# Performance work log

Measured on AMD Instinct MI355X. Metric: run time of the kernel, lower is better.

The kernel has to match this reference:

```python
import jax, jax.numpy as jnp
import numpy as np

EMB_DIM = 1024
N_HEADS = 16
HEAD_DIM = EMB_DIM // N_HEADS
WINDOW = 128
B, T = 4, 2048


def setup_inputs() -> dict:
    key = jax.random.key(0)
    k1, k2, k3 = jax.random.split(key, 3)
    x = jax.random.normal(k1, (B, T, EMB_DIM), dtype=jnp.float32)
    # nn.Linear weights: stored as [out, in], applied as x @ W^T
    s1 = 1.0 / np.sqrt(EMB_DIM)
    w_qkv = jax.random.uniform(k2, (3 * EMB_DIM, EMB_DIM), jnp.float32, -s1, s1)
    w_out = jax.random.uniform(k3, (EMB_DIM, EMB_DIM), jnp.float32, -s1, s1)
    return {"x": x, "w_qkv": w_qkv, "w_out": w_out}


def reference(x, w_qkv, w_out):
    Bs, Ts, C = x.shape
    scale = HEAD_DIM ** -0.5
    qkv = x @ w_qkv.T                                   # [B,T,3C]
    qkv = qkv.reshape(Bs, Ts, 3, N_HEADS, HEAD_DIM)
    qkv = jnp.transpose(qkv, (2, 0, 3, 1, 4))           # [3,B,H,T,D]
    q, k, v = qkv[0], qkv[1], qkv[2]
    scores = jnp.einsum('bhtd,bhsd->bhts', q, k) * scale  # [B,H,T,T]
    i = jnp.arange(Ts)[:, None]
    j = jnp.arange(Ts)[None, :]
    # causal AND within sliding window: i - WINDOW <= j <= i
    allowed = (j <= i) & (j >= i - WINDOW)               # [T,T] bool
    scores = jnp.where(allowed[None, None], scores, -jnp.inf)
    attn = jax.nn.softmax(scores, axis=-1)
    out = jnp.einsum('bhts,bhsd->bhtd', attn, v)         # [B,H,T,D]
    out = jnp.transpose(out, (0, 2, 1, 3)).reshape(Bs, Ts, C)
    return out @ w_out.T
```

## Files before the change

kernel.cpp:

```cpp
#include <hip/hip_runtime.h>
#include <hip/hip_bf16.h>
#include <stdint.h>

typedef __attribute__((ext_vector_type(8))) short bf16x8;
typedef __attribute__((ext_vector_type(4))) float f32x4;
typedef __attribute__((ext_vector_type(4))) unsigned short u16x4;

#define B_ 4
#define T_ 2048
#define C_ 1024
#define H_ 16
#define D_ 64

__device__ __forceinline__ unsigned short f2bf(float f) {
  union { float f; uint32_t u; } v; v.f = f;
  uint32_t u = v.u;
  uint32_t r = (u + 0x7FFFu + ((u >> 16) & 1u)) >> 16;
  return (unsigned short)r;
}

__global__ void __launch_bounds__(256) cast_all(const float* __restrict__ x,
                                                const float* __restrict__ wqkv,
                                                const float* __restrict__ wout,
                                                unsigned short* __restrict__ xb,
                                                unsigned short* __restrict__ wqkvb,
                                                unsigned short* __restrict__ woutb) {
  int bid = blockIdx.x;
  const float* src; unsigned short* dst; int i;
  if (bid < 8192)       { src = x;    dst = xb;    i = bid * 256 + threadIdx.x; }
  else if (bid < 11264) { src = wqkv; dst = wqkvb; i = (bid - 8192) * 256 + threadIdx.x; }
  else                  { src = wout; dst = woutb; i = (bid - 11264) * 256 + threadIdx.x; }
  float4 f = ((const float4*)src)[i];
  u16x4 o;
  o[0] = f2bf(f.x); o[1] = f2bf(f.y); o[2] = f2bf(f.z); o[3] = f2bf(f.w);
  ((u16x4*)dst)[i] = o;
}

__global__ void __launch_bounds__(256, 2) gemm_qkv(const unsigned short* __restrict__ A,
                                                   const unsigned short* __restrict__ Bm,
                                                   unsigned short* __restrict__ qb,
                                                   unsigned short* __restrict__ kb,
                                                   unsigned short* __restrict__ vb) {
  __shared__ short lds[24576];
  const int tid = threadIdx.x;
  const int bm = blockIdx.y * 256;
  const int bn = blockIdx.x * 128;

  const int wave = tid >> 6;
  const int l = tid & 63;
  const int wm = wave >> 1, wn = wave & 1;
  const int lm = l & 15, lq = l >> 4;
  const int lr = l >> 2;
  const int lc = (l & 3) << 3;

  f32x4 acc[8][4];
#pragma unroll
  for (int i = 0; i < 8; i++)
#pragma unroll
    for (int j = 0; j < 4; j++) acc[i][j] = (f32x4){0.f, 0.f, 0.f, 0.f};

  const unsigned short* gs[6];
  int ldo[6];
#pragma unroll
  for (int i = 0; i < 6; i++) {
    int c = wave * 6 + i;
    if (c < 16) {
      gs[i] = A + (size_t)(bm + 16 * c + lr) * 1024 + lc;
      ldo[i] = c * 512;
    } else {
      gs[i] = Bm + (size_t)(bn + 16 * (c - 16) + lr) * 1024 + lc;
      ldo[i] = 8192 + (c - 16) * 512;
    }
  }

#define STAGE(curb, kk)                                                          \
  do {                                                                           \
    _Pragma("unroll")                                                            \
    for (int i = 0; i < 6; i++) {                                                \
      __builtin_amdgcn_global_load_lds(                                          \
          (__attribute__((address_space(1))) void*)(uintptr_t)(const void*)(gs[i] + (kk)), \
          (__attribute__((address_space(3))) void*)(lds + ldo[i] + (curb) * 12288),        \
          16, 0, 0);                                                             \
    }                                                                            \
  } while (0)

  STAGE(0, 0);
  int cur = 0;
  __syncthreads();

  for (int k0 = 0; k0 < 1024; k0 += 32) {
    if (k0 + 32 < 1024) STAGE(cur ^ 1, k0 + 32);
    const short* As_ = lds + cur * 12288;
    const short* Bs_ = lds + cur * 12288 + 8192;
    bf16x8 Bf[4];
#pragma unroll
    for (int j = 0; j < 4; j++)
      Bf[j] = *(const bf16x8*)&Bs_[(wn * 64 + 16 * j + lm) * 32 + 8 * lq];
#pragma unroll
    for (int h = 0; h < 2; h++) {
      bf16x8 Af[4];
#pragma unroll
      for (int i = 0; i < 4; i++)
        Af[i] = *(const bf16x8*)&As_[(wm * 128 + 64 * h + 16 * i + lm) * 32 + 8 * lq];
#pragma unroll
      for (int i = 0; i < 4; i++)
#pragma unroll
        for (int j = 0; j < 4; j++)
          acc[4 * h + i][j] =
              __builtin_amdgcn_mfma_f32_16x16x32_bf16(Af[i], Bf[j], acc[4 * h + i][j], 0, 0, 0);
    }
    __syncthreads();
    cur ^= 1;
  }
#undef STAGE

  if (bn >= 2048) {
#pragma unroll
    for (int h = 0; h < 2; h++)
#pragma unroll
      for (int i = 0; i < 4; i++)
#pragma unroll
        for (int j = 0; j < 4; j++) {
          int m0 = bm + wm * 128 + 64 * h + 16 * i + 4 * lq;
          int n = (bn - 2048) + wn * 64 + 16 * j + lm;
          int hh = n >> 6, d = n & 63;
          int b = m0 >> 11, t = m0 & 2047;
          u16x4 o;
#pragma unroll
          for (int r = 0; r < 4; r++) o[r] = f2bf(acc[4 * h + i][j][r]);
          *(u16x4*)&vb[(((size_t)(b * 16 + hh)) * 64 + d) * 2048 + t] = o;
        }
  } else {
#pragma unroll
    for (int p = 0; p < 2; ++p) {
      if (p) __syncthreads();
      if (wm == p) {
#pragma unroll
        for (int h = 0; h < 2; h++)
#pragma unroll
          for (int i = 0; i < 4; i++)
#pragma unroll
            for (int j = 0; j < 4; j++)
#pragma unroll
              for (int r = 0; r < 4; r++)
                lds[(64 * h + 16 * i + 4 * lq + r) * 132 + wn * 64 + 16 * j + lm] =
                    (short)f2bf(acc[4 * h + i][j][r]);
      }
      __syncthreads();
#pragma unroll
      for (int k = 0; k < 8; k++) {
        int c = tid + 256 * k;
        int row = c >> 4;
        int col = (c & 15) << 3;
        bf16x8 v = *(const bf16x8*)&lds[row * 132 + col];
        int m = bm + 128 * p + row, n = bn + col;
        int which = n >> 10, rem = n & 1023;
        int hh = rem >> 6, d = rem & 63;
        int b = m >> 11, t = m & 2047;
        unsigned short* dst = (which == 0) ? qb : kb;
        *(bf16x8*)&dst[(((size_t)(b * 16 + hh)) * 2048 + t) * 64 + d] = v;
      }
    }
  }
}

__global__ void __launch_bounds__(256) gemm_out(const unsigned short* __restrict__ A,
                                                const unsigned short* __restrict__ Bm,
                                                float* __restrict__ fo) {
  __shared__ short lds[16384];
  const int tid = threadIdx.x;
  const int bm = blockIdx.y * 128;
  const int bn = blockIdx.x * 128;
  const int wave = tid >> 6;
  const int l = tid & 63;
  const int wm = wave >> 1, wn = wave & 1;
  const int lm = l & 15, lq = l >> 4;
  const int lr = l >> 2;
  const int lc = (l & 3) << 3;

  f32x4 acc[4][4];
#pragma unroll
  for (int i = 0; i < 4; i++)
#pragma unroll
    for (int j = 0; j < 4; j++) acc[i][j] = (f32x4){0.f, 0.f, 0.f, 0.f};

  const unsigned short* gsrc[4];
  int ldoff[4];
#pragma unroll
  for (int i = 0; i < 4; i++) {
    int c = wave * 4 + i;
    if (c < 8) {
      gsrc[i] = A + (size_t)(bm + 16 * c + lr) * 1024 + lc;
      ldoff[i] = (16 * c) * 32;
    } else {
      gsrc[i] = Bm + (size_t)(bn + 16 * (c - 8) + lr) * 1024 + lc;
      ldoff[i] = 8192 + (16 * (c - 8)) * 32;
    }
  }

#define STAGE(curb, kk)                                                          \
  do {                                                                           \
    _Pragma("unroll")                                                            \
    for (int i = 0; i < 4; i++) {                                                \
      __builtin_amdgcn_global_load_lds(                                          \
          (__attribute__((address_space(1))) void*)(uintptr_t)(const void*)(gsrc[i] + (kk)), \
          (__attribute__((address_space(3))) void*)(lds + ldoff[i] + (curb) * 4096),         \
          16, 0, 0);                                                             \
    }                                                                            \
  } while (0)

  STAGE(0, 0);
  int cur = 0;
  __syncthreads();

  for (int k0 = 0; k0 < 1024; k0 += 32) {
    if (k0 + 32 < 1024) STAGE(cur ^ 1, k0 + 32);
    bf16x8 af[4], bfr[4];
#pragma unroll
    for (int i = 0; i < 4; i++)
      af[i] = *(const bf16x8*)&lds[cur * 4096 + (wm * 64 + 16 * i + lm) * 32 + 8 * lq];
#pragma unroll
    for (int j = 0; j < 4; j++)
      bfr[j] = *(const bf16x8*)&lds[8192 + cur * 4096 + (wn * 64 + 16 * j + lm) * 32 + 8 * lq];
#pragma unroll
    for (int i = 0; i < 4; i++)
#pragma unroll
      for (int j = 0; j < 4; j++)
        acc[i][j] = __builtin_amdgcn_mfma_f32_16x16x32_bf16(af[i], bfr[j], acc[i][j], 0, 0, 0);
    __syncthreads();
    cur ^= 1;
  }
#undef STAGE

#pragma unroll
  for (int i = 0; i < 4; i++)
#pragma unroll
    for (int j = 0; j < 4; j++)
#pragma unroll
      for (int r = 0; r < 4; r++) {
        int m = bm + wm * 64 + 16 * i + 4 * lq + r;
        int n = bn + wn * 64 + 16 * j + lm;
        fo[(size_t)m * 1024 + n] = acc[i][j][r];
      }
}

__global__ void __launch_bounds__(256, 4) attn_swa(const unsigned short* __restrict__ Qb,
                                                   const unsigned short* __restrict__ Kb,
                                                   const unsigned short* __restrict__ Vt,
                                                   unsigned short* __restrict__ Ob) {
  __shared__ short P[4][16 * 48];
  const int wv = threadIdx.x >> 6;
  const int l = threadIdx.x & 63;
  const int wid = blockIdx.x * 4 + wv;
  const int bh = wid >> 6;
  const int t0 = (wid & 63) << 5;
  const int lm = l & 15, lq = l >> 4;
  const size_t base = (size_t)bh * (T_ * D_);

  bf16x8 qf[2][2];
#pragma unroll
  for (int qt = 0; qt < 2; qt++) {
    qf[qt][0] = *(const bf16x8*)(Qb + base + (size_t)(t0 + 16 * qt + lm) * 64 + 8 * lq);
    qf[qt][1] = *(const bf16x8*)(Qb + base + (size_t)(t0 + 16 * qt + lm) * 64 + 32 + 8 * lq);
  }

  float mst[2] = {-1e30f, -1e30f}, lst[2] = {0.f, 0.f};
  f32x4 Oa[2][4];
#pragma unroll
  for (int qt = 0; qt < 2; qt++)
#pragma unroll
    for (int jt = 0; jt < 4; jt++) Oa[qt][jt] = (f32x4){0.f, 0.f, 0.f, 0.f};

  const float cs = 0.125f * 1.44269504f;
  int jstart = t0 - 128; if (jstart < 0) jstart = 0;

  for (int j0 = jstart; j0 < t0 + 32; j0 += 32) {
    bf16x8 ka[2][2];
#pragma unroll
    for (int hh = 0; hh < 2; hh++) {
      int kr = j0 + 16 * hh + lm;
      ka[hh][0] = *(const bf16x8*)(Kb + base + (size_t)kr * 64 + 8 * lq);
      ka[hh][1] = *(const bf16x8*)(Kb + base + (size_t)kr * 64 + 32 + 8 * lq);
    }
    bf16x8 vf[4];
#pragma unroll
    for (int jt = 0; jt < 4; jt++)
      vf[jt] = *(const bf16x8*)(Vt + base + (size_t)(16 * jt + lm) * 2048 + j0 + 8 * lq);

#pragma unroll
    for (int qt = 0; qt < 2; qt++) {
      const int t0q = t0 + 16 * qt;
      const int t = t0q + lm;
      f32x4 s0 = (f32x4){0.f, 0.f, 0.f, 0.f}, s1 = (f32x4){0.f, 0.f, 0.f, 0.f};
      s0 = __builtin_amdgcn_mfma_f32_16x16x32_bf16(ka[0][0], qf[qt][0], s0, 0, 0, 0);
      s0 = __builtin_amdgcn_mfma_f32_16x16x32_bf16(ka[0][1], qf[qt][1], s0, 0, 0, 0);
      s1 = __builtin_amdgcn_mfma_f32_16x16x32_bf16(ka[1][0], qf[qt][0], s1, 0, 0, 0);
      s1 = __builtin_amdgcn_mfma_f32_16x16x32_bf16(ka[1][1], qf[qt][1], s1, 0, 0, 0);
      float sv[8];
      float m2 = -1e30f;
#pragma unroll
      for (int hh = 0; hh < 2; hh++)
#pragma unroll
        for (int r = 0; r < 4; r++) {
          int k = j0 + 16 * hh + 4 * lq + r;
          float x = (hh ? s1[r] : s0[r]) * cs;
          bool okm = (k <= t) && (k + 128 >= t);
          sv[hh * 4 + r] = okm ? x : -1e30f;
          m2 = fmaxf(m2, sv[hh * 4 + r]);
        }
      m2 = fmaxf(m2, __shfl_xor(m2, 16));
      m2 = fmaxf(m2, __shfl_xor(m2, 32));
      float mn = fmaxf(mst[qt], m2);
      float a = __builtin_amdgcn_exp2f(mst[qt] - mn);
      float ps = 0.f;
#pragma unroll
      for (int i = 0; i < 8; i++) {
        sv[i] = (sv[i] > -1e29f) ? __builtin_amdgcn_exp2f(sv[i] - mn) : 0.f;
        ps += sv[i];
      }
      ps += __shfl_xor(ps, 16);
      ps += __shfl_xor(ps, 32);
      lst[qt] = lst[qt] * a + ps;
      mst[qt] = mn;
#pragma unroll
      for (int hh = 0; hh < 2; hh++) {
        u16x4 pk;
#pragma unroll
        for (int r = 0; r < 4; r++) pk[r] = f2bf(sv[hh * 4 + r]);
        *(u16x4*)&P[wv][lm * 48 + 16 * hh + 4 * lq] = pk;
      }
      float al[4];
#pragma unroll
      for (int r = 0; r < 4; r++) al[r] = __shfl(a, 4 * lq + r);
#pragma unroll
      for (int jt = 0; jt < 4; jt++)
#pragma unroll
        for (int r = 0; r < 4; r++) Oa[qt][jt][r] *= al[r];
      bf16x8 pa = *(const bf16x8*)&P[wv][lm * 48 + 8 * lq];
#pragma unroll
      for (int jt = 0; jt < 4; jt++)
        Oa[qt][jt] = __builtin_amdgcn_mfma_f32_16x16x32_bf16(pa, vf[jt], Oa[qt][jt], 0, 0, 0);
    }
  }
  const int b = bh >> 4, h = bh & 15;
#pragma unroll
  for (int qt = 0; qt < 2; qt++) {
    float inv = 1.0f / lst[qt];
    float invl[4];
#pragma unroll
    for (int r = 0; r < 4; r++) invl[r] = __shfl(inv, 4 * lq + r);
#pragma unroll
    for (int r = 0; r < 4; r++) {
      int t = t0 + 16 * qt + 4 * lq + r;
#pragma unroll
      for (int jt = 0; jt < 4; jt++) {
        int c = h * 64 + 16 * jt + lm;
        Ob[((size_t)(b * T_ + t)) * 1024 + c] = f2bf(Oa[qt][jt][r] * invl[r]);
      }
    }
  }
}

extern "C" void kernel_launch(void* const* d_in, const int* in_sizes, int n_in,
                              void* d_out, int out_size, void* d_ws, size_t ws_size,
                              hipStream_t stream) {
  const float* x = (const float*)d_in[0];
  const float* w_qkv = (const float*)d_in[1];
  const float* w_out = (const float*)d_in[2];
  float* out = (float*)d_out;

  unsigned short* xb = (unsigned short*)d_ws;
  unsigned short* wqkvb = xb + (size_t)8192 * 1024;
  unsigned short* woutb = wqkvb + (size_t)3072 * 1024;
  unsigned short* qb = woutb + (size_t)1024 * 1024;
  unsigned short* kb = qb + (size_t)64 * 2048 * 64;
  unsigned short* vb = kb + (size_t)64 * 2048 * 64;

  cast_all<<<12288, 256, 0, stream>>>(x, w_qkv, w_out, xb, wqkvb, woutb);

  gemm_qkv<<<dim3(24, 32), 256, 0, stream>>>(xb, wqkvb, qb, kb, vb);

  attn_swa<<<1024, 256, 0, stream>>>(qb, kb, vb, xb);

  gemm_out<<<dim3(8, 64), 256, 0, stream>>>(xb, woutb, out);
}
```

Before: 216.4 us.

## Rewrite QKV GEMM as 8-wave 256x256 tile with 4-stage LDS pipeline

The QKV projection GEMM moves from 256-thread blocks with 256x128 tiles and double buffering to 512-thread blocks with 256x256 tiles. It uses a 4-deep LDS ring buffer whose A and B stages are issued at separate points in the loop, controlled with explicit vmcnt/lgkmcnt waits, raw s_barrier, sched_barrier fences and setprio around the MFMA bursts. The goal is more operand reuse per LDS load and better overlap of global-to-LDS copies with matrix math. In exchange it uses 128KB of LDS per block, which may limit occupancy to one block per CU, and relies on fragile hand-counted wait counts.

```diff
diff --git a/kernel.cpp b/kernel.cpp
--- a/kernel.cpp
+++ b/kernel.cpp
@@ -36,22 +36,20 @@
   ((u16x4*)dst)[i] = o;
 }
 
-__global__ void __launch_bounds__(256, 2) gemm_qkv(const unsigned short* __restrict__ A,
-                                                   const unsigned short* __restrict__ Bm,
-                                                   unsigned short* __restrict__ qb,
-                                                   unsigned short* __restrict__ kb,
-                                                   unsigned short* __restrict__ vb) {
-  __shared__ short lds[24576];
+__global__ void __launch_bounds__(512, 2) gemm_qkv8(const unsigned short* __restrict__ A,
+                                                    const unsigned short* __restrict__ Bm,
+                                                    unsigned short* __restrict__ qb,
+                                                    unsigned short* __restrict__ kb,
+                                                    unsigned short* __restrict__ vb) {
+  __shared__ short lds[65536];
   const int tid = threadIdx.x;
   const int bm = blockIdx.y * 256;
-  const int bn = blockIdx.x * 128;
-
+  const int bn = blockIdx.x * 256;
   const int wave = tid >> 6;
   const int l = tid & 63;
-  const int wm = wave >> 1, wn = wave & 1;
+  const int wr = wave >> 2;
+  const int wc = wave & 3;
   const int lm = l & 15, lq = l >> 4;
-  const int lr = l >> 2;
-  const int lc = (l & 3) << 3;
 
   f32x4 acc[8][4];
 #pragma unroll
@@ -59,109 +57,135 @@
 #pragma unroll
     for (int j = 0; j < 4; j++) acc[i][j] = (f32x4){0.f, 0.f, 0.f, 0.f};
 
-  const unsigned short* gs[6];
-  int ldo[6];
-#pragma unroll
-  for (int i = 0; i < 6; i++) {
-    int c = wave * 6 + i;
-    if (c < 16) {
-      gs[i] = A + (size_t)(bm + 16 * c + lr) * 1024 + lc;
-      ldo[i] = c * 512;
-    } else {
-      gs[i] = Bm + (size_t)(bn + 16 * (c - 16) + lr) * 1024 + lc;
-      ldo[i] = 8192 + (c - 16) * 512;
-    }
-  }
-
-#define STAGE(curb, kk)                                                          \
+  const unsigned short* gA[2];
+  const unsigned short* gB[2];
+  int dA[2], dB[2];
+#pragma unroll
+  for (int i = 0; i < 2; i++) {
+    int c = i * 512 + tid;
+    gA[i] = A + (size_t)(bm + (c >> 2)) * 1024 + (c & 3) * 8;
+    gB[i] = Bm + (size_t)(bn + (c >> 2)) * 1024 + (c & 3) * 8;
+    dA[i] = c * 8;
+    dB[i] = 8192 + c * 8;
+  }
+
+#define STA(t)                                                                   \
   do {                                                                           \
     _Pragma("unroll")                                                            \
-    for (int i = 0; i < 6; i++) {                                                \
+    for (int i = 0; i < 2; i++)                                                  \
       __builtin_amdgcn_global_load_lds(                                          \
-          (__attribute__((address_space(1))) void*)(uintptr_t)(const void*)(gs[i] + (kk)), \
-          (__attribute__((address_space(3))) void*)(lds + ldo[i] + (curb) * 12288),        \
+          (__attribute__((address_space(1))) void*)(uintptr_t)(const void*)(gA[i] + (t) * 32), \
+          (__attribute__((address_space(3))) void*)(lds + ((t) & 3) * 16384 + dA[i]),          \
           16, 0, 0);                                                             \
-    }                                                                            \
   } while (0)
-
-  STAGE(0, 0);
-  int cur = 0;
-  __syncthreads();
-
-  for (int k0 = 0; k0 < 1024; k0 += 32) {
-    if (k0 + 32 < 1024) STAGE(cur ^ 1, k0 + 32);
-    const short* As_ = lds + cur * 12288;
-    const short* Bs_ = lds + cur * 12288 + 8192;
-    bf16x8 Bf[4];
-#pragma unroll
-    for (int j = 0; j < 4; j++)
-      Bf[j] = *(const bf16x8*)&Bs_[(wn * 64 + 16 * j + lm) * 32 + 8 * lq];
-#pragma unroll
-    for (int h = 0; h < 2; h++) {
-      bf16x8 Af[4];
-#pragma unroll
-      for (int i = 0; i < 4; i++)
-        Af[i] = *(const bf16x8*)&As_[(wm * 128 + 64 * h + 16 * i + lm) * 32 + 8 * lq];
-#pragma unroll
-      for (int i = 0; i < 4; i++)
-#pragma unroll
-        for (int j = 0; j < 4; j++)
-          acc[4 * h + i][j] =
-              __builtin_amdgcn_mfma_f32_16x16x32_bf16(Af[i], Bf[j], acc[4 * h + i][j], 0, 0, 0);
-    }
-    __syncthreads();
-    cur ^= 1;
-  }
-#undef STAGE
+#define STB(t)                                                                   \
+  do {                                                                           \
+    _Pragma("unroll")                                                            \
+    for (int i = 0; i < 2; i++)                                                  \
+      __builtin_amdgcn_global_load_lds(                                          \
+          (__attribute__((address_space(1))) void*)(uintptr_t)(const void*)(gB[i] + (t) * 32), \
+          (__attribute__((address_space(3))) void*)(lds + ((t) & 3) * 16384 + dB[i]),          \
+          16, 0, 0);                                                             \
+  } while (0)
+#define FENCE() __builtin_amdgcn_sched_barrier(0)
+
+  STA(0); STB(0); STA(1); STB(1);
+  FENCE();
+
+  for (int t = 0; t < 32; ++t) {
+    const short* Sa = lds + (t & 3) * 16384;
+    const short* Sb = Sa + 8192;
+    if (t + 2 < 32) STA(t + 2);
+    FENCE();
+    if (t <= 29)      asm volatile("s_waitcnt vmcnt(6)" ::: "memory");
+    else if (t == 30) asm volatile("s_waitcnt vmcnt(4)" ::: "memory");
+    else              asm volatile("s_waitcnt vmcnt(0)" ::: "memory");
+    __builtin_amdgcn_s_barrier();
+    FENCE();
+    bf16x8 Af[8], Bf[2];
+#pragma unroll
+    for (int mi = 0; mi < 8; mi++)
+      Af[mi] = *(const bf16x8*)&Sa[(wr * 128 + 16 * mi + lm) * 32 + 8 * lq];
+#pragma unroll
+    for (int nj = 0; nj < 2; nj++)
+      Bf[nj] = *(const bf16x8*)&Sb[(wc * 64 + 16 * nj + lm) * 32 + 8 * lq];
+    asm volatile("s_waitcnt lgkmcnt(0)" ::: "memory");
+    FENCE();
+    __builtin_amdgcn_s_setprio(1);
+#pragma unroll
+    for (int mi = 0; mi < 8; mi++)
+#pragma unroll
+      for (int nj = 0; nj < 2; nj++)
+        acc[mi][nj] = __builtin_amdgcn_mfma_f32_16x16x32_bf16(Af[mi], Bf[nj], acc[mi][nj], 0, 0, 0);
+    __builtin_amdgcn_s_setprio(0);
+    FENCE();
+    if (t + 2 < 32) STB(t + 2);
+    FENCE();
+    __builtin_amdgcn_s_barrier();
+    FENCE();
+    bf16x8 Bg[2];
+#pragma unroll
+    for (int nj = 0; nj < 2; nj++)
+      Bg[nj] = *(const bf16x8*)&Sb[(wc * 64 + 16 * (nj + 2) + lm) * 32 + 8 * lq];
+    asm volatile("s_waitcnt lgkmcnt(0)" ::: "memory");
+    FENCE();
+    __builtin_amdgcn_s_setprio(1);
+#pragma unroll
+    for (int mi = 0; mi < 8; mi++)
+#pragma unroll
+      for (int nj = 0; nj < 2; nj++)
+        acc[mi][2 + nj] = __builtin_amdgcn_mfma_f32_16x16x32_bf16(Af[mi], Bg[nj], acc[mi][2 + nj], 0, 0, 0);
+    __builtin_amdgcn_s_setprio(0);
+    FENCE();
+  }
+#undef STA
+#undef STB
 
   if (bn >= 2048) {
 #pragma unroll
-    for (int h = 0; h < 2; h++)
-#pragma unroll
-      for (int i = 0; i < 4; i++)
-#pragma unroll
-        for (int j = 0; j < 4; j++) {
-          int m0 = bm + wm * 128 + 64 * h + 16 * i + 4 * lq;
-          int n = (bn - 2048) + wn * 64 + 16 * j + lm;
-          int hh = n >> 6, d = n & 63;
-          int b = m0 >> 11, t = m0 & 2047;
-          u16x4 o;
-#pragma unroll
-          for (int r = 0; r < 4; r++) o[r] = f2bf(acc[4 * h + i][j][r]);
-          *(u16x4*)&vb[(((size_t)(b * 16 + hh)) * 64 + d) * 2048 + t] = o;
-        }
+    for (int mi = 0; mi < 8; mi++)
+#pragma unroll
+      for (int nj = 0; nj < 4; nj++) {
+        int m0 = bm + wr * 128 + 16 * mi + 4 * lq;
+        int n = (bn - 2048) + wc * 64 + 16 * nj + lm;
+        int hh = n >> 6, d = n & 63;
+        int b = m0 >> 11, tt = m0 & 2047;
+        u16x4 o;
+#pragma unroll
+        for (int r = 0; r < 4; r++) o[r] = f2bf(acc[mi][nj][r]);
+        *(u16x4*)&vb[(((size_t)(b * 16 + hh)) * 64 + d) * 2048 + tt] = o;
+      }
   } else {
 #pragma unroll
     for (int p = 0; p < 2; ++p) {
-      if (p) __syncthreads();
-      if (wm == p) {
-#pragma unroll
-        for (int h = 0; h < 2; h++)
-#pragma unroll
-          for (int i = 0; i < 4; i++)
-#pragma unroll
-            for (int j = 0; j < 4; j++)
-#pragma unroll
-              for (int r = 0; r < 4; r++)
-                lds[(64 * h + 16 * i + 4 * lq + r) * 132 + wn * 64 + 16 * j + lm] =
-                    (short)f2bf(acc[4 * h + i][j][r]);
-      }
       __syncthreads();
+      if (wr == p) {
+#pragma unroll
+        for (int mi = 0; mi < 8; mi++)
+#pragma unroll
+          for (int nj = 0; nj < 4; nj++)
+#pragma unroll
+            for (int r = 0; r < 4; r++)
+              lds[(16 * mi + 4 * lq + r) * 264 + wc * 64 + 16 * nj + lm] =
+                  (short)f2bf(acc[mi][nj][r]);
+      }
+      __syncthreads();
 #pragma unroll
       for (int k = 0; k < 8; k++) {
-        int c = tid + 256 * k;
-        int row = c >> 4;
-        int col = (c & 15) << 3;
-        bf16x8 v = *(const bf16x8*)&lds[row * 132 + col];
+        int c = tid + 512 * k;
+        int row = c >> 5;
+        int col = (c & 31) << 3;
+        bf16x8 v = *(const bf16x8*)&lds[row * 264 + col];
         int m = bm + 128 * p + row, n = bn + col;
         int which = n >> 10, rem = n & 1023;
         int hh = rem >> 6, d = rem & 63;
-        int b = m >> 11, t = m & 2047;
+        int b = m >> 11, tt = m & 2047;
         unsigned short* dst = (which == 0) ? qb : kb;
-        *(bf16x8*)&dst[(((size_t)(b * 16 + hh)) * 2048 + t) * 64 + d] = v;
+        *(bf16x8*)&dst[(((size_t)(b * 16 + hh)) * 2048 + tt) * 64 + d] = v;
       }
     }
   }
+#undef FENCE
 }
 
 __global__ void __launch_bounds__(256) gemm_out(const unsigned short* __restrict__ A,
@@ -378,7 +402,7 @@
 
   cast_all<<<12288, 256, 0, stream>>>(x, w_qkv, w_out, xb, wqkvb, woutb);
 
-  gemm_qkv<<<dim3(24, 32), 256, 0, stream>>>(xb, wqkvb, qb, kb, vb);
+  gemm_qkv8<<<dim3(12, 32), 512, 0, stream>>>(xb, wqkvb, qb, kb, vb);
 
   attn_swa<<<1024, 256, 0, stream>>>(qb, kb, vb, xb);
 
```

New measurement: 218.8 us. Within noise of the previous version (+1.1%).

## Use 128x128 tiles with 64-wide K steps in both GEMMs

Applied to the files above, without the earlier changes.

The QKV GEMM drops from 256x128 to 128x128 block tiles, which doubles the grid to 1536 blocks and removes the two-pass epilogue. Both GEMMs now stage two 32-wide K slices per iteration into a larger LDS buffer (64 KB), so there is one barrier per 64 of K instead of per 32. This trades A-tile reuse and LDS occupancy for more parallelism and fewer synchronisations.

```diff
diff --git a/kernel.cpp b/kernel.cpp
--- a/kernel.cpp
+++ b/kernel.cpp
@@ -36,14 +36,14 @@
   ((u16x4*)dst)[i] = o;
 }
 
-__global__ void __launch_bounds__(256, 2) gemm_qkv(const unsigned short* __restrict__ A,
-                                                   const unsigned short* __restrict__ Bm,
-                                                   unsigned short* __restrict__ qb,
-                                                   unsigned short* __restrict__ kb,
-                                                   unsigned short* __restrict__ vb) {
-  __shared__ short lds[24576];
+__global__ void __launch_bounds__(256) gemm_qkv(const unsigned short* __restrict__ A,
+                                                const unsigned short* __restrict__ Bm,
+                                                unsigned short* __restrict__ qb,
+                                                unsigned short* __restrict__ kb,
+                                                unsigned short* __restrict__ vb) {
+  __shared__ short lds[32768];
   const int tid = threadIdx.x;
-  const int bm = blockIdx.y * 256;
+  const int bm = blockIdx.y * 128;
   const int bn = blockIdx.x * 128;
 
   const int wave = tid >> 6;
@@ -53,113 +53,105 @@
   const int lr = l >> 2;
   const int lc = (l & 3) << 3;
 
-  f32x4 acc[8][4];
-#pragma unroll
-  for (int i = 0; i < 8; i++)
+  f32x4 acc[4][4];
+#pragma unroll
+  for (int i = 0; i < 4; i++)
 #pragma unroll
     for (int j = 0; j < 4; j++) acc[i][j] = (f32x4){0.f, 0.f, 0.f, 0.f};
 
-  const unsigned short* gs[6];
-  int ldo[6];
-#pragma unroll
-  for (int i = 0; i < 6; i++) {
-    int c = wave * 6 + i;
-    if (c < 16) {
-      gs[i] = A + (size_t)(bm + 16 * c + lr) * 1024 + lc;
-      ldo[i] = c * 512;
+  const unsigned short* gsrc[4];
+  int ldoff[4];
+#pragma unroll
+  for (int i = 0; i < 4; i++) {
+    int c = wave * 4 + i;
+    if (c < 8) {
+      gsrc[i] = A + (size_t)(bm + 16 * c + lr) * 1024 + lc;
+      ldoff[i] = c * 512;
     } else {
-      gs[i] = Bm + (size_t)(bn + 16 * (c - 16) + lr) * 1024 + lc;
-      ldo[i] = 8192 + (c - 16) * 512;
-    }
-  }
-
-#define STAGE(curb, kk)                                                          \
+      gsrc[i] = Bm + (size_t)(bn + 16 * (c - 8) + lr) * 1024 + lc;
+      ldoff[i] = 16384 + (c - 8) * 512;
+    }
+  }
+
+#define STAGE(q, kk)                                                             \
   do {                                                                           \
     _Pragma("unroll")                                                            \
-    for (int i = 0; i < 6; i++) {                                                \
+    for (int i = 0; i < 4; i++) {                                                \
       __builtin_amdgcn_global_load_lds(                                          \
-          (__attribute__((address_space(1))) void*)(uintptr_t)(const void*)(gs[i] + (kk)), \
-          (__attribute__((address_space(3))) void*)(lds + ldo[i] + (curb) * 12288),        \
+          (__attribute__((address_space(1))) void*)(uintptr_t)(const void*)(gsrc[i] + (kk)), \
+          (__attribute__((address_space(3))) void*)(lds + ldoff[i] + (q) * 4096),            \
           16, 0, 0);                                                             \
     }                                                                            \
   } while (0)
 
   STAGE(0, 0);
-  int cur = 0;
+  STAGE(1, 32);
   __syncthreads();
 
-  for (int k0 = 0; k0 < 1024; k0 += 32) {
-    if (k0 + 32 < 1024) STAGE(cur ^ 1, k0 + 32);
-    const short* As_ = lds + cur * 12288;
-    const short* Bs_ = lds + cur * 12288 + 8192;
-    bf16x8 Bf[4];
-#pragma unroll
-    for (int j = 0; j < 4; j++)
-      Bf[j] = *(const bf16x8*)&Bs_[(wn * 64 + 16 * j + lm) * 32 + 8 * lq];
-#pragma unroll
-    for (int h = 0; h < 2; h++) {
-      bf16x8 Af[4];
+  for (int kk = 0; kk < 1024; kk += 64) {
+    const int cp = (kk >> 6) & 1;
+    if (kk + 64 < 1024) {
+      STAGE(2 * (1 - cp), kk + 64);
+      STAGE(2 * (1 - cp) + 1, kk + 96);
+    }
+#pragma unroll
+    for (int sub = 0; sub < 2; sub++) {
+      const int q = 2 * cp + sub;
+      const short* As_ = lds + q * 4096;
+      const short* Bs_ = lds + 16384 + q * 4096;
+      bf16x8 af[4], bfr[4];
 #pragma unroll
       for (int i = 0; i < 4; i++)
-        Af[i] = *(const bf16x8*)&As_[(wm * 128 + 64 * h + 16 * i + lm) * 32 + 8 * lq];
+        af[i] = *(const bf16x8*)&As_[(wm * 64 + 16 * i + lm) * 32 + 8 * lq];
+#pragma unroll
+      for (int j = 0; j < 4; j++)
+        bfr[j] = *(const bf16x8*)&Bs_[(wn * 64 + 16 * j + lm) * 32 + 8 * lq];
 #pragma unroll
       for (int i = 0; i < 4; i++)
 #pragma unroll
         for (int j = 0; j < 4; j++)
-          acc[4 * h + i][j] =
-              __builtin_amdgcn_mfma_f32_16x16x32_bf16(Af[i], Bf[j], acc[4 * h + i][j], 0, 0, 0);
+          acc[i][j] = __builtin_amdgcn_mfma_f32_16x16x32_bf16(af[i], bfr[j], acc[i][j], 0, 0, 0);
     }
     __syncthreads();
-    cur ^= 1;
   }
 #undef STAGE
 
   if (bn >= 2048) {
 #pragma unroll
-    for (int h = 0; h < 2; h++)
-#pragma unroll
-      for (int i = 0; i < 4; i++)
-#pragma unroll
-        for (int j = 0; j < 4; j++) {
-          int m0 = bm + wm * 128 + 64 * h + 16 * i + 4 * lq;
-          int n = (bn - 2048) + wn * 64 + 16 * j + lm;
-          int hh = n >> 6, d = n & 63;
-          int b = m0 >> 11, t = m0 & 2047;
-          u16x4 o;
-#pragma unroll
-          for (int r = 0; r < 4; r++) o[r] = f2bf(acc[4 * h + i][j][r]);
-          *(u16x4*)&vb[(((size_t)(b * 16 + hh)) * 64 + d) * 2048 + t] = o;
-        }
+    for (int i = 0; i < 4; i++)
+#pragma unroll
+      for (int j = 0; j < 4; j++) {
+        int m0 = bm + wm * 64 + 16 * i + 4 * lq;
+        int n = (bn - 2048) + wn * 64 + 16 * j + lm;
+        int h = n >> 6, d = n & 63;
+        int b = m0 >> 11, t = m0 & 2047;
+        u16x4 o;
+#pragma unroll
+        for (int r = 0; r < 4; r++) o[r] = f2bf(acc[i][j][r]);
+        *(u16x4*)&vb[(((size_t)(b * 16 + h)) * 64 + d) * 2048 + t] = o;
+      }
   } else {
 #pragma unroll
-    for (int p = 0; p < 2; ++p) {
-      if (p) __syncthreads();
-      if (wm == p) {
-#pragma unroll
-        for (int h = 0; h < 2; h++)
-#pragma unroll
-          for (int i = 0; i < 4; i++)
-#pragma unroll
-            for (int j = 0; j < 4; j++)
-#pragma unroll
-              for (int r = 0; r < 4; r++)
-                lds[(64 * h + 16 * i + 4 * lq + r) * 132 + wn * 64 + 16 * j + lm] =
-                    (short)f2bf(acc[4 * h + i][j][r]);
-      }
-      __syncthreads();
-#pragma unroll
-      for (int k = 0; k < 8; k++) {
-        int c = tid + 256 * k;
-        int row = c >> 4;
-        int col = (c & 15) << 3;
-        bf16x8 v = *(const bf16x8*)&lds[row * 132 + col];
-        int m = bm + 128 * p + row, n = bn + col;
-        int which = n >> 10, rem = n & 1023;
-        int hh = rem >> 6, d = rem & 63;
-        int b = m >> 11, t = m & 2047;
-        unsigned short* dst = (which == 0) ? qb : kb;
-        *(bf16x8*)&dst[(((size_t)(b * 16 + hh)) * 2048 + t) * 64 + d] = v;
-      }
+    for (int i = 0; i < 4; i++)
+#pragma unroll
+      for (int j = 0; j < 4; j++)
+#pragma unroll
+        for (int r = 0; r < 4; r++)
+          lds[(wm * 64 + 16 * i + 4 * lq + r) * 132 + wn * 64 + 16 * j + lm] =
+              (short)f2bf(acc[i][j][r]);
+    __syncthreads();
+#pragma unroll
+    for (int k = 0; k < 8; k++) {
+      int c = tid + 256 * k;
+      int row = c >> 4;
+      int col = (c & 15) << 3;
+      bf16x8 v = *(const bf16x8*)&lds[row * 132 + col];
+      int m = bm + row, n = bn + col;
+      int which = n >> 10, rem = n & 1023;
+      int h = rem >> 6, d = rem & 63;
+      int b = m >> 11, t = m & 2047;
+      unsigned short* dst = (which == 0) ? qb : kb;
+      *(bf16x8*)&dst[(((size_t)(b * 16 + h)) * 2048 + t) * 64 + d] = v;
     }
   }
 }
@@ -167,7 +159,7 @@
 __global__ void __launch_bounds__(256) gemm_out(const unsigned short* __restrict__ A,
                                                 const unsigned short* __restrict__ Bm,
                                                 float* __restrict__ fo) {
-  __shared__ short lds[16384];
+  __shared__ short lds[32768];
   const int tid = threadIdx.x;
   const int bm = blockIdx.y * 128;
   const int bn = blockIdx.x * 128;
@@ -191,44 +183,53 @@
     int c = wave * 4 + i;
     if (c < 8) {
       gsrc[i] = A + (size_t)(bm + 16 * c + lr) * 1024 + lc;
-      ldoff[i] = (16 * c) * 32;
+      ldoff[i] = c * 512;
     } else {
       gsrc[i] = Bm + (size_t)(bn + 16 * (c - 8) + lr) * 1024 + lc;
-      ldoff[i] = 8192 + (16 * (c - 8)) * 32;
-    }
-  }
-
-#define STAGE(curb, kk)                                                          \
+      ldoff[i] = 16384 + (c - 8) * 512;
+    }
+  }
+
+#define STAGE(q, kk)                                                             \
   do {                                                                           \
     _Pragma("unroll")                                                            \
     for (int i = 0; i < 4; i++) {                                                \
       __builtin_amdgcn_global_load_lds(                                          \
           (__attribute__((address_space(1))) void*)(uintptr_t)(const void*)(gsrc[i] + (kk)), \
-          (__attribute__((address_space(3))) void*)(lds + ldoff[i] + (curb) * 4096),         \
+          (__attribute__((address_space(3))) void*)(lds + ldoff[i] + (q) * 4096),            \
           16, 0, 0);                                                             \
     }                                                                            \
   } while (0)
 
   STAGE(0, 0);
-  int cur = 0;
+  STAGE(1, 32);
   __syncthreads();
 
-  for (int k0 = 0; k0 < 1024; k0 += 32) {
-    if (k0 + 32 < 1024) STAGE(cur ^ 1, k0 + 32);
-    bf16x8 af[4], bfr[4];
-#pragma unroll
-    for (int i = 0; i < 4; i++)
-      af[i] = *(const bf16x8*)&lds[cur * 4096 + (wm * 64 + 16 * i + lm) * 32 + 8 * lq];
-#pragma unroll
-    for (int j = 0; j < 4; j++)
-      bfr[j] = *(const bf16x8*)&lds[8192 + cur * 4096 + (wn * 64 + 16 * j + lm) * 32 + 8 * lq];
-#pragma unroll
-    for (int i = 0; i < 4; i++)
+  for (int kk = 0; kk < 1024; kk += 64) {
+    const int cp = (kk >> 6) & 1;
+    if (kk + 64 < 1024) {
+      STAGE(2 * (1 - cp), kk + 64);
+      STAGE(2 * (1 - cp) + 1, kk + 96);
+    }
+#pragma unroll
+    for (int sub = 0; sub < 2; sub++) {
+      const int q = 2 * cp + sub;
+      const short* As_ = lds + q * 4096;
+      const short* Bs_ = lds + 16384 + q * 4096;
+      bf16x8 af[4], bfr[4];
+#pragma unroll
+      for (int i = 0; i < 4; i++)
+        af[i] = *(const bf16x8*)&As_[(wm * 64 + 16 * i + lm) * 32 + 8 * lq];
 #pragma unroll
       for (int j = 0; j < 4; j++)
-        acc[i][j] = __builtin_amdgcn_mfma_f32_16x16x32_bf16(af[i], bfr[j], acc[i][j], 0, 0, 0);
+        bfr[j] = *(const bf16x8*)&Bs_[(wn * 64 + 16 * j + lm) * 32 + 8 * lq];
+#pragma unroll
+      for (int i = 0; i < 4; i++)
+#pragma unroll
+        for (int j = 0; j < 4; j++)
+          acc[i][j] = __builtin_amdgcn_mfma_f32_16x16x32_bf16(af[i], bfr[j], acc[i][j], 0, 0, 0);
+    }
     __syncthreads();
-    cur ^= 1;
   }
 #undef STAGE
 
@@ -378,7 +379,7 @@
 
   cast_all<<<12288, 256, 0, stream>>>(x, w_qkv, w_out, xb, wqkvb, woutb);
 
-  gemm_qkv<<<dim3(24, 32), 256, 0, stream>>>(xb, wqkvb, qb, kb, vb);
+  gemm_qkv<<<dim3(24, 64), 256, 0, stream>>>(xb, wqkvb, qb, kb, vb);
 
   attn_swa<<<1024, 256, 0, stream>>>(qb, kb, vb, xb);
 
```

New measurement: 205.0 us. 1.06x faster.
